# Performance work log

Hardware: AMD Instinct MI355X
Metric: run time of the kernel (lower is better)

## Reference

```python
import jax, jax.numpy as jnp
import numpy as np

S, B, DIN, DBERT, H, L = 128, 32, 256, 768, 512, 2
NT_POS, NT_MORPH = 32, 64


def setup_inputs() -> dict:
    key = jax.random.key(0)
    ks = iter(jax.random.split(key, 32))
    def rn(shape, s=0.1):
        return jax.random.normal(next(ks), shape, dtype=jnp.float32) * s
    D0 = DIN + DBERT  # 1024 == 2*H, so per-layer LSTM weights stack cleanly
    return {
        "src_segments": rn((S, B, DIN), 1.0),
        "bert_encodings": rn((B, DBERT), 1.0),
        "labels_pos": jax.random.randint(next(ks), (S, B), 0, NT_POS, dtype=jnp.int32),
        "labels_morph": jax.random.randint(next(ks), (S, B), 0, NT_MORPH, dtype=jnp.int32),
        # stacked LSTM params: [layer, direction, ...], PyTorch gate order i,f,g,o
        "w_ih": rn((L, 2, 4 * H, D0)),
        "w_hh": rn((L, 2, 4 * H, H)),
        "b_ih": rn((L, 2, 4 * H)),
        "b_hh": rn((L, 2, 4 * H)),
        "head_w_pos": rn((NT_POS, 2 * H)),
        "head_b_pos": rn((NT_POS,)),
        "head_w_morph": rn((NT_MORPH, 2 * H)),
        "head_b_morph": rn((NT_MORPH,)),
        "start_pos": rn((NT_POS,)), "end_pos": rn((NT_POS,)), "trans_pos": rn((NT_POS, NT_POS)),
        "start_morph": rn((NT_MORPH,)), "end_morph": rn((NT_MORPH,)), "trans_morph": rn((NT_MORPH, NT_MORPH)),
    }


def _run_dir(x, w_ih, w_hh, b):
    # x: [S, B, D]; one LSTM direction via scan over time
    bsz, hd = x.shape[1], w_hh.shape[1]
    def step(carry, xt):
        h, c = carry
        g = xt @ w_ih.T + h @ w_hh.T + b  # [B, 4H]
        i, f, gg, o = jnp.split(g, 4, axis=-1)
        c = jax.nn.sigmoid(f) * c + jax.nn.sigmoid(i) * jnp.tanh(gg)
        h = jax.nn.sigmoid(o) * jnp.tanh(c)
        return (h, c), h
    init = (jnp.zeros((bsz, hd), x.dtype), jnp.zeros((bsz, hd), x.dtype))
    _, hs = jax.lax.scan(step, init, x)
    return hs


def _bilstm(x, w_ih, w_hh, b_ih, b_hh):
    out = x
    for l in range(w_ih.shape[0]):
        b = b_ih[l] + b_hh[l]
        fwd = _run_dir(out, w_ih[l, 0], w_hh[l, 0], b[0])
        bwd = _run_dir(out[::-1], w_ih[l, 1], w_hh[l, 1], b[1])[::-1]
        out = jnp.concatenate([fwd, bwd], axis=-1)  # [S, B, 2H]
    return out


def _crf_ll(em, tags, start, trans, end):
    # torchcrf log-likelihood, mask=None, reduction='sum'. em: [S,B,K], tags: [S,B]
    bsz = em.shape[1]
    first = start[tags[0]] + em[0, jnp.arange(bsz), tags[0]]
    em_sc = jnp.take_along_axis(em, tags[..., None], axis=2)[..., 0]  # [S,B]
    num = first + trans[tags[:-1], tags[1:]].sum(0) + em_sc[1:].sum(0) + end[tags[-1]]
    def step(alpha, et):  # alpha: [B,K]
        return jax.nn.logsumexp(alpha[:, :, None] + trans[None], axis=1) + et, None
    alpha, _ = jax.lax.scan(step, start[None, :] + em[0], em[1:])
    den = jax.nn.logsumexp(alpha + end[None, :], axis=1)
    return jnp.sum(num - den)


def reference(src_segments, bert_encodings, labels_pos, labels_morph,
              w_ih, w_hh, b_ih, b_hh,
              head_w_pos, head_b_pos, head_w_morph, head_b_morph,
              start_pos, end_pos, trans_pos, start_morph, end_morph, trans_morph):
    # bert encodings are repeated over seq and concatenated on features
    bert = jnp.broadcast_to(bert_encodings[None], (src_segments.shape[0],) + bert_encodings.shape)
    emb = jnp.concatenate([src_segments, bert], axis=-1)  # dropout p=0 -> identity
    out = _bilstm(emb, w_ih, w_hh, b_ih, b_hh)            # [S,B,2H]
    feat_pos = out @ head_w_pos.T + head_b_pos            # [S,B,32]
    feat_morph = out @ head_w_morph.T + head_b_morph      # [S,B,64]
    ll = (_crf_ll(feat_pos, labels_pos, start_pos, trans_pos, end_pos)
          + _crf_ll(feat_morph, labels_morph, start_morph, trans_morph, end_morph))
    return -ll  # loss = -sum_f crf_f(emissions_f, labels_f)
```

## Files before the change

### kernel.cpp

```cpp
#include <hip/hip_runtime.h>


typedef unsigned short u16;
typedef unsigned int u32;
typedef unsigned long long u64;
typedef __attribute__((ext_vector_type(8))) __bf16 bf16x8;
typedef __attribute__((ext_vector_type(4))) float floatx4;

typedef const __attribute__((address_space(1))) u32 gu32;
typedef __attribute__((address_space(3))) u32 lu32;

static __device__ __forceinline__ u16 f2bf(float f) {
  u32 u = __float_as_uint(f);
  u += 0x7fffu + ((u >> 16) & 1u);
  return (u16)(u >> 16);
}
static __device__ __forceinline__ u64 pack4(float4 v) {
  return (u64)f2bf(v.x) | ((u64)f2bf(v.y) << 16) |
         ((u64)f2bf(v.z) << 32) | ((u64)f2bf(v.w) << 48);
}
static __device__ __forceinline__ float bf2f(u32 bits) {
  return __uint_as_float(bits << 16);
}
static __device__ __forceinline__ float sigf(float x) {
  return 1.0f / (1.0f + __expf(-x));
}
static __device__ __forceinline__ float tanh_(float x) {
  return 1.0f - 2.0f / (1.0f + __expf(2.0f * x));
}
static __device__ __forceinline__ floatx4 mfma16(bf16x8 a, bf16x8 b, floatx4 c) {
  return __builtin_amdgcn_mfma_f32_16x16x32_bf16(a, b, c, 0, 0, 0);
}
static __device__ __forceinline__ u64 aload64(const u64* p) {
  return __hip_atomic_load((u64*)p, __ATOMIC_RELAXED, __HIP_MEMORY_SCOPE_AGENT);
}
static __device__ __forceinline__ void astore64(u64* p, u64 v) {
  __hip_atomic_store(p, v, __ATOMIC_RELAXED, __HIP_MEMORY_SCOPE_AGENT);
}
static __device__ __forceinline__ void gload16(const u16* g, u16* lds_base) {
  __builtin_amdgcn_global_load_lds((gu32*)g, (lu32*)lds_base, 16, 0, 0);
}

__global__ __launch_bounds__(256) void prep_kernel(
    const float* __restrict__ w_ih, const float* __restrict__ w_hh,
    const float* __restrict__ b_ih, const float* __restrict__ b_hh,
    const float* __restrict__ src,  const float* __restrict__ bert,
    const float* __restrict__ hwp,  const float* __restrict__ hbp,
    const float* __restrict__ hwm,  const float* __restrict__ hbm,
    u16* __restrict__ Wsrc, u16* __restrict__ Wbert, u16* __restrict__ Wih1,
    u16* __restrict__ Whh,  u16* __restrict__ SrcBf, u16* __restrict__ BertBf,
    u16* __restrict__ Wheads, float* __restrict__ b0sum, float* __restrict__ b1sum,
    float* __restrict__ hb, float* __restrict__ dout,
    u64* __restrict__ out0s, u64* __restrict__ out1s)
{
  const int A4 = 1048576;
  const int B4 = 1048576;
  const int C4 = 1048576;
  const int D4 = 262144;
  const int E4 = 6144;
  const int F4 = 24576;
  const int G4 = 2048;
  const int H4 = 24;
  const int NI = 2097152;
  const int TOTAL = A4 + B4 + C4 + D4 + E4 + F4 + G4 + H4 + 1 + NI;
  for (int i = blockIdx.x * 256 + threadIdx.x; i < TOTAL; i += gridDim.x * 256) {
    int x = i;
    if (x < A4) {
      const int e = x * 4, c = e & 1023, r = e >> 10;
      const u64 pk = pack4(*(const float4*)&w_ih[e]);
      if (c < 256) *(u64*)&Wsrc[r * 256 + c] = pk;
      else         *(u64*)&Wbert[r * 768 + (c - 256)] = pk;
      continue;
    }
    x -= A4;
    if (x < B4) {
      *(u64*)&Wih1[x * 4] = pack4(*(const float4*)&w_ih[4194304 + x * 4]);
      continue;
    }
    x -= B4;
    if (x < C4) {
      *(u64*)&Whh[x * 4] = pack4(*(const float4*)&w_hh[x * 4]);
      continue;
    }
    x -= C4;
    if (x < D4) {
      *(u64*)&SrcBf[x * 4] = pack4(*(const float4*)&src[x * 4]);
      continue;
    }
    x -= D4;
    if (x < E4) {
      *(u64*)&BertBf[x * 4] = pack4(*(const float4*)&bert[x * 4]);
      continue;
    }
    x -= E4;
    if (x < F4) {
      const int e = x * 4;
      const float4 v = (e < 32768) ? *(const float4*)&hwp[e]
                                   : *(const float4*)&hwm[e - 32768];
      *(u64*)&Wheads[e] = pack4(v);
      continue;
    }
    x -= F4;
    if (x < G4) {
      const int e = x * 4;
      const float4 a = *(const float4*)&b_ih[e];
      const float4 b = *(const float4*)&b_hh[e];
      const float4 v = {a.x + b.x, a.y + b.y, a.z + b.z, a.w + b.w};
      if (e < 4096) *(float4*)&b0sum[e] = v;
      else          *(float4*)&b1sum[e - 4096] = v;
      continue;
    }
    x -= G4;
    if (x < H4) {
      const int e = x * 4;
      const float4 v = (e < 32) ? *(const float4*)&hbp[e]
                                : *(const float4*)&hbm[e - 32];
      *(float4*)&hb[e] = v;
      continue;
    }
    x -= H4;
    if (x == 0) { dout[0] = 0.f; continue; }
    x -= 1;
    if (x < 1048576) out0s[x] = ~0ULL;
    else             out1s[x - 1048576] = ~0ULL;
  }
}

__global__ __launch_bounds__(256) void gemm_nt(
    const u16* __restrict__ A, int lda,
    const u16* __restrict__ B, int ldb,
    float* __restrict__ C, int ldc,
    int M, int N, int K,
    const float* __restrict__ bias_n,
    const float* __restrict__ auxBN, int auxld,
    int mode)
{
  __shared__ __align__(16) u16 As[128 * 64];
  __shared__ __align__(16) u16 Bs[128 * 64];
  const int m0 = blockIdx.y * 128, n0 = blockIdx.x * 128;
  const int tid = threadIdx.x;
  const int wv = tid >> 6, ln = tid & 63;
  const int wm = wv & 1, wn = wv >> 1;
  const int q = ln >> 4, l15 = ln & 15;
  floatx4 acc[4][4];
#pragma unroll
  for (int a = 0; a < 4; ++a)
#pragma unroll
    for (int b2 = 0; b2 < 4; ++b2) acc[a][b2] = (floatx4){0.f, 0.f, 0.f, 0.f};

  for (int kk = 0; kk < K; kk += 64) {
    __syncthreads();
#pragma unroll
    for (int j = 0; j < 4; ++j) {
      const int idx = j * 256 + tid;
      const int r = idx >> 3;
      const int cc = (idx & 7) ^ (r & 7);
      const int cb = __builtin_amdgcn_readfirstlane((j * 256 + wv * 64) * 8);
      const int ra = min(m0 + r, M - 1);
      gload16(&A[(long)ra * lda + kk + cc * 8], &As[cb]);
      const int rb = min(n0 + r, N - 1);
      gload16(&B[(long)rb * ldb + kk + cc * 8], &Bs[cb]);
    }
    __syncthreads();
#pragma unroll
    for (int ks = 0; ks < 2; ++ks) {
      bf16x8 af[4], bf[4];
#pragma unroll
      for (int im = 0; im < 4; ++im) {
        const int r = wm * 64 + im * 16 + l15;
        const int slot = (ks * 4 + q) ^ (r & 7);
        af[im] = *(const bf16x8*)&As[r * 64 + slot * 8];
      }
#pragma unroll
      for (int jn = 0; jn < 4; ++jn) {
        const int r = wn * 64 + jn * 16 + l15;
        const int slot = (ks * 4 + q) ^ (r & 7);
        bf[jn] = *(const bf16x8*)&Bs[r * 64 + slot * 8];
      }
#pragma unroll
      for (int im = 0; im < 4; ++im)
#pragma unroll
        for (int jn = 0; jn < 4; ++jn)
          acc[im][jn] = mfma16(af[im], bf[jn], acc[im][jn]);
    }
  }
  if (mode == 0) {
#pragma unroll
    for (int im = 0; im < 4; ++im)
#pragma unroll
      for (int jn = 0; jn < 4; ++jn) {
        const int n = n0 + wn * 64 + jn * 16 + l15;
        if (n < N) {
          const float badd = bias_n ? bias_n[n] : 0.f;
#pragma unroll
          for (int rg = 0; rg < 4; ++rg) {
            const int m = m0 + wm * 64 + im * 16 + q * 4 + rg;
            if (m < M) {
              float v = acc[im][jn][rg] + badd;
              if (auxBN) v += auxBN[(long)(m & 31) * auxld + n];
              C[(long)m * ldc + n] = v;
            }
          }
        }
      }
  } else {
    u64* G = (u64*)C;
#pragma unroll
    for (int im = 0; im < 4; ++im)
#pragma unroll
      for (int jn = 0; jn < 4; ++jn) {
        const int n = n0 + wn * 64 + jn * 16 + l15;
        const int dirsel = n >> 11, nn = n & 2047;
        const int gt = nn >> 9, u = nn & 511;
        const int ub = u >> 4, low = u & 15;
        const int wvl = low >> 2, jl = low & 3;
        const int l15l = gt * 4 + jl;
        const int m = m0 + wm * 64 + im * 16 + q * 4;
        const int s = m >> 5, b0 = m & 31;
        const int mh = b0 >> 4, qq = (b0 >> 2) & 3;
        const float badd = bias_n ? bias_n[n] : 0.f;
        u64 pk = 0;
#pragma unroll
        for (int rg = 0; rg < 4; ++rg) {
          float v = acc[im][jn][rg] + badd;
          if (auxBN) v += auxBN[(long)(b0 + rg) * auxld + n];
          pk |= (u64)f2bf(v) << (16 * rg);
        }
        G[(((((long)dirsel * 128 + s) * 2 + mh) * 32 + ub) * 4 + wvl) * 64
          + l15l * 4 + qq] = pk;
      }
  }
}

__global__ __launch_bounds__(256, 1) void lstm_rec(
    const u16* __restrict__ gates,
    u16* __restrict__ out,
    const u16* __restrict__ whh)
{
  __shared__ __align__(16) u16 h_lds[16 * 512];
  __shared__ float gsc[4][16][17];
  const int bid = blockIdx.x;
  const int dir = bid >> 6;
  const int mh = (bid >> 5) & 1;
  const int ub = bid & 31;
  const int u0 = ub * 16;
  const int tid = threadIdx.x;
  const int wv = tid >> 6;
  const int ln = tid & 63;
  const int q = ln >> 4, l15 = ln & 15;

  const int gate_r = (l15 >> 2) * 512 + u0 + wv * 4 + (l15 & 3);

  bf16x8 bfrag[16];
  {
    const u16* wp = whh + ((long)dir * 2048 + gate_r) * 512 + q * 8;
#pragma unroll
    for (int ks = 0; ks < 16; ++ks)
      bfrag[ks] = *(const bf16x8*)(wp + ks * 32);
  }

  float c = 0.f;
  const int b_glob = mh * 16 + l15;

  const u64* gbase = (const u64*)gates
      + ((((long)dir * 128 * 2 + mh) * 32 + ub) * 4 + wv) * 64 + l15 * 4 + q;

  u64 gcur = gbase[(long)(dir ? 127 : 0) * 16384];
  u64 gnext = 0;

  for (int t = 0; t < 128; ++t) {
    const int s = dir ? (127 - t) : t;
    if (t < 127) {
      const int sn = dir ? (126 - t) : (t + 1);
      gnext = gbase[(long)sn * 16384];
    }
    floatx4 acc = (floatx4){0.f, 0.f, 0.f, 0.f};
    if (t > 0) {
      const int sp = dir ? (s + 1) : (s - 1);
      const u64* ubp = (const u64*)(out + (((long)sp * 32 + mh * 16) * 1024 + (long)dir * 512));
      u64 v8[8];
#pragma unroll
      for (int j = 0; j < 8; ++j) {
        const int idx = j * 256 + tid;
        const int r = idx >> 7, c4 = idx & 127;
        v8[j] = aload64(ubp + (long)r * 256 + c4);
      }
      while (true) {
        bool bad = false;
#pragma unroll
        for (int j = 0; j < 8; ++j) bad |= ((v8[j] & 0xffffULL) == 0xffffULL);
        if (!bad) break;
#pragma unroll
        for (int j = 0; j < 8; ++j) {
          if ((v8[j] & 0xffffULL) == 0xffffULL) {
            const int idx = j * 256 + tid;
            const int r = idx >> 7, c4 = idx & 127;
            v8[j] = aload64(ubp + (long)r * 256 + c4);
          }
        }
      }
#pragma unroll
      for (int j = 0; j < 8; ++j) {
        const int idx = j * 256 + tid;
        const int r = idx >> 7, c4 = idx & 127;
        const int cc8 = c4 >> 1, hf = c4 & 1;
        *(u64*)&h_lds[r * 512 + ((cc8 ^ (r & 7)) << 3) + (hf << 2)] = v8[j];
      }
      __syncthreads();
      floatx4 acc1 = (floatx4){0.f, 0.f, 0.f, 0.f};
      floatx4 acc2 = (floatx4){0.f, 0.f, 0.f, 0.f};
      floatx4 acc3 = (floatx4){0.f, 0.f, 0.f, 0.f};
#pragma unroll
      for (int ks = 0; ks < 16; ks += 4) {
        const int slot0 = (ks * 4 + q) ^ (l15 & 7);
        bf16x8 a0 = *(const bf16x8*)&h_lds[l15 * 512 + slot0 * 8];
        acc = mfma16(a0, bfrag[ks], acc);
        const int slot1 = ((ks + 1) * 4 + q) ^ (l15 & 7);
        bf16x8 a1 = *(const bf16x8*)&h_lds[l15 * 512 + slot1 * 8];
        acc1 = mfma16(a1, bfrag[ks + 1], acc1);
        const int slot2 = ((ks + 2) * 4 + q) ^ (l15 & 7);
        bf16x8 a2 = *(const bf16x8*)&h_lds[l15 * 512 + slot2 * 8];
        acc2 = mfma16(a2, bfrag[ks + 2], acc2);
        const int slot3 = ((ks + 3) * 4 + q) ^ (l15 & 7);
        bf16x8 a3 = *(const bf16x8*)&h_lds[l15 * 512 + slot3 * 8];
        acc3 = mfma16(a3, bfrag[ks + 3], acc3);
      }
      acc += acc1;
      acc2 += acc3;
      acc += acc2;
    }
#pragma unroll
    for (int rg = 0; rg < 4; ++rg)
      gsc[wv][q * 4 + rg][l15] = acc[rg] + bf2f((u32)((gcur >> (16 * rg)) & 0xffffu));
    const float gi = gsc[wv][l15][q];
    const float gf = gsc[wv][l15][4 + q];
    const float gg = gsc[wv][l15][8 + q];
    const float go = gsc[wv][l15][12 + q];
    const float iv = sigf(gi), fv = sigf(gf), gv = tanh_(gg), ov = sigf(go);
    c = fv * c + iv * gv;
    const float h = ov * tanh_(c);
    const u32 hv = (u32)f2bf(h);
    const u32 p1 = (u32)__shfl_xor((int)hv, 16);
    const u32 lo32 = hv | (p1 << 16);
    const u64 w64 = (u64)lo32 |
                    ((u64)(u32)__shfl_xor((int)lo32, 32) << 32);
    if (q == 0)
      astore64(
          (u64*)&out[((long)s * 32 + b_glob) * 1024 + dir * 512 + u0 + wv * 4],
          w64);
    gcur = gnext;
  }
}

template <int K>
static __device__ void crf_body(const float* __restrict__ feat, int off,
                                const int* __restrict__ labels, int b,
                                const float* __restrict__ start,
                                const float* __restrict__ end_,
                                const float* __restrict__ trans,
                                float* __restrict__ outp,
                                float* transT, float (*alpha)[64],
                                float* red)
{
  const int tid = threadIdx.x;
  for (int i = tid; i < K * K; i += 256) {
    int kk = i / K, kp2 = i % K;
    transT[kp2 * 65 + kk] = trans[i];
  }
  if (tid < K) alpha[0][tid] = start[tid] + feat[b * 96 + off + tid];
  __syncthreads();
  constexpr int Kq = K / 4;
  const int kp = tid >> 2, k4 = tid & 3;
  const bool act = kp < K;
  int p = 0;
  for (int s = 1; s < 128; ++s) {
    float x[Kq];
    float mx = -3e38f;
    if (act) {
      const float* tr = &transT[kp * 65 + k4 * Kq];
      const float* al = &alpha[p][k4 * Kq];
#pragma unroll
      for (int i2 = 0; i2 < Kq; ++i2) { x[i2] = al[i2] + tr[i2]; mx = fmaxf(mx, x[i2]); }
    }
    mx = fmaxf(mx, __shfl_xor(mx, 1));
    mx = fmaxf(mx, __shfl_xor(mx, 2));
    float ss = 0.f;
    if (act) {
#pragma unroll
      for (int i2 = 0; i2 < Kq; ++i2) ss += __expf(x[i2] - mx);
    }
    ss += __shfl_xor(ss, 1);
    ss += __shfl_xor(ss, 2);
    if (act && k4 == 0)
      alpha[p ^ 1][kp] = mx + __logf(ss) + feat[(s * 32 + b) * 96 + off + kp];
    __syncthreads();
    p ^= 1;
  }
  if (tid < 128) {
    const int tg = labels[tid * 32 + b];
    float term = feat[(tid * 32 + b) * 96 + off + tg];
    if (tid == 0) term += start[tg];
    else          term += trans[labels[(tid - 1) * 32 + b] * K + tg];
    if (tid == 127) term += end_[tg];
    red[tid] = term;
  }
  __syncthreads();
  if (tid == 0) {
    float num = 0.f;
    for (int i = 0; i < 128; ++i) num += red[i];
    float mx = -3e38f;
    for (int k = 0; k < K; ++k) mx = fmaxf(mx, alpha[p][k] + end_[k]);
    float ss = 0.f;
    for (int k = 0; k < K; ++k) ss += __expf(alpha[p][k] + end_[k] - mx);
    const float den = mx + __logf(ss);
    atomicAdd(outp, den - num);
  }
}

__global__ __launch_bounds__(256) void crf_kernel(
    const float* __restrict__ feat,
    const int* __restrict__ labp, const int* __restrict__ labm,
    const float* __restrict__ stp, const float* __restrict__ enp, const float* __restrict__ trp,
    const float* __restrict__ stm, const float* __restrict__ enm, const float* __restrict__ trm,
    float* __restrict__ outp)
{
  __shared__ float transT[64 * 65];
  __shared__ float alpha[2][64];
  __shared__ float red[128];
  const int task = blockIdx.x >> 5, b = blockIdx.x & 31;
  if (task == 0) crf_body<32>(feat, 0,  labp, b, stp, enp, trp, outp, transT, alpha, red);
  else           crf_body<64>(feat, 32, labm, b, stm, enm, trm, outp, transT, alpha, red);
}

extern "C" void kernel_launch(void* const* d_in, const int* in_sizes, int n_in,
                              void* d_out, int out_size, void* d_ws, size_t ws_size,
                              hipStream_t stream) {
  const float* src  = (const float*)d_in[0];
  const float* bert = (const float*)d_in[1];
  const int*   labp = (const int*)d_in[2];
  const int*   labm = (const int*)d_in[3];
  const float* w_ih = (const float*)d_in[4];
  const float* w_hh = (const float*)d_in[5];
  const float* b_ih = (const float*)d_in[6];
  const float* b_hh = (const float*)d_in[7];
  const float* hwp  = (const float*)d_in[8];
  const float* hbp  = (const float*)d_in[9];
  const float* hwm  = (const float*)d_in[10];
  const float* hbm  = (const float*)d_in[11];
  const float* stp  = (const float*)d_in[12];
  const float* enp  = (const float*)d_in[13];
  const float* trp  = (const float*)d_in[14];
  const float* stm  = (const float*)d_in[15];
  const float* enm  = (const float*)d_in[16];
  const float* trm  = (const float*)d_in[17];

  char* ws = (char*)d_ws;
  u16*   Wsrc     = (u16*)(ws + 0);
  u16*   Wbert    = (u16*)(ws + 2097152);
  u16*   Wih1     = (u16*)(ws + 8388608);
  u16*   Whh      = (u16*)(ws + 16777216);
  u16*   SrcBf    = (u16*)(ws + 25165824);
  u16*   BertBf   = (u16*)(ws + 27262976);
  u16*   Wheads   = (u16*)(ws + 27312128);
  float* b0sum    = (float*)(ws + 27508736);
  float* b1sum    = (float*)(ws + 27525120);
  float* hb       = (float*)(ws + 27541504);
  float* bertpart = (float*)(ws + 27542272);
  float* feat     = (float*)(ws + 28066560);
  u16*   out0     = (u16*)(ws + 29639424);
  u16*   out1     = (u16*)(ws + 38028032);
  u16*   gates    = (u16*)(ws + 46416640);
  float* dout     = (float*)d_out;

  hipLaunchKernelGGL(prep_kernel, dim3(2048), dim3(256), 0, stream,
      w_ih, w_hh, b_ih, b_hh, src, bert, hwp, hbp, hwm, hbm,
      Wsrc, Wbert, Wih1, Whh, SrcBf, BertBf, Wheads, b0sum, b1sum, hb, dout,
      (u64*)out0, (u64*)out1);

  hipLaunchKernelGGL(gemm_nt, dim3(32, 1), dim3(256), 0, stream,
      BertBf, 768, Wbert, 768, bertpart, 4096, 32, 4096, 768,
      b0sum, (const float*)nullptr, 0, 0);

  hipLaunchKernelGGL(gemm_nt, dim3(32, 32), dim3(256), 0, stream,
      SrcBf, 256, Wsrc, 256, (float*)gates, 0, 4096, 4096, 256,
      (const float*)nullptr, bertpart, 4096, 1);

  {
    const u16* g = gates; u16* o = out0; const u16* wh = Whh;
    void* args[] = {&g, &o, &wh};
    if (hipLaunchCooperativeKernel(reinterpret_cast<void*>(&lstm_rec),
                                   dim3(128), dim3(256), args, 0, stream)
        != hipSuccess) {
      hipLaunchKernelGGL(lstm_rec, dim3(128), dim3(256), 0, stream, g, o, wh);
    }
  }

  hipLaunchKernelGGL(gemm_nt, dim3(32, 32), dim3(256), 0, stream,
      out0, 1024, Wih1, 1024, (float*)gates, 0, 4096, 4096, 1024,
      b1sum, (const float*)nullptr, 0, 1);

  {
    const u16* g = gates; u16* o = out1; const u16* wh = Whh + 2L * 2048 * 512;
    void* args[] = {&g, &o, &wh};
    if (hipLaunchCooperativeKernel(reinterpret_cast<void*>(&lstm_rec),
                                   dim3(128), dim3(256), args, 0, stream)
        != hipSuccess) {
      hipLaunchKernelGGL(lstm_rec, dim3(128), dim3(256), 0, stream, g, o, wh);
    }
  }

  hipLaunchKernelGGL(gemm_nt, dim3(1, 32), dim3(256), 0, stream,
      out1, 1024, Wheads, 1024, feat, 96, 4096, 96, 1024,
      hb, (const float*)nullptr, 0, 0);

  hipLaunchKernelGGL(crf_kernel, dim3(64), dim3(256), 0, stream,
      feat, labp, labm, stp, enp, trp, stm, enm, trm, dout);
}
```

Baseline: 872.3 us.

## Repartition LSTM recurrence into 16 blocks of 1024 threads covering full batch

The recurrent LSTM kernel is restructured from 128 blocks of 256 threads, each handling 16 hidden units for half the batch, to 16 blocks of 1024 threads. Each block now handles 64 hidden units for all 32 batch rows, reusing each W_hh fragment for two MFMA row tiles. The aim is to cut redundant weight residency and the number of blocks polling the cross-block h spin-wait each step. In exchange, each step runs on far fewer CUs, with larger blocks, a bigger LDS footprint and serialized gate processing for the two batch halves.

```diff
diff --git a/kernel.cpp b/kernel.cpp
--- a/kernel.cpp
+++ b/kernel.cpp
@@ -232,24 +232,22 @@
   }
 }
 
-__global__ __launch_bounds__(256, 1) void lstm_rec(
+__global__ __launch_bounds__(1024, 1) void lstm_rec2(
     const u16* __restrict__ gates,
     u16* __restrict__ out,
     const u16* __restrict__ whh)
 {
-  __shared__ __align__(16) u16 h_lds[16 * 512];
-  __shared__ float gsc[4][16][17];
+  __shared__ __align__(16) u16 h_lds[32 * 512];
+  __shared__ float gsc[16][16][17];
   const int bid = blockIdx.x;
-  const int dir = bid >> 6;
-  const int mh = (bid >> 5) & 1;
-  const int ub = bid & 31;
-  const int u0 = ub * 16;
+  const int dir = bid >> 3;
+  const int u8b = bid & 7;
   const int tid = threadIdx.x;
-  const int wv = tid >> 6;
+  const int w = tid >> 6;
   const int ln = tid & 63;
   const int q = ln >> 4, l15 = ln & 15;
 
-  const int gate_r = (l15 >> 2) * 512 + u0 + wv * 4 + (l15 & 3);
+  const int gate_r = (l15 >> 2) * 512 + u8b * 64 + w * 4 + (l15 & 3);
 
   bf16x8 bfrag[16];
   {
@@ -259,96 +257,113 @@
       bfrag[ks] = *(const bf16x8*)(wp + ks * 32);
   }
 
-  float c = 0.f;
-  const int b_glob = mh * 16 + l15;
-
-  const u64* gbase = (const u64*)gates
-      + ((((long)dir * 128 * 2 + mh) * 32 + ub) * 4 + wv) * 64 + l15 * 4 + q;
-
-  u64 gcur = gbase[(long)(dir ? 127 : 0) * 16384];
-  u64 gnext = 0;
+  float c0 = 0.f, c1 = 0.f;
+
+  const u64* gb = (const u64*)gates + (long)dir * 2097152
+      + (long)(u8b * 4 + (w >> 2)) * 256 + (w & 3) * 64 + l15 * 4 + q;
+
+  const long s0 = (long)(dir ? 127 : 0) * 16384;
+  u64 gcur0 = gb[s0];
+  u64 gcur1 = gb[s0 + 8192];
+  u64 gnext0 = 0, gnext1 = 0;
 
   for (int t = 0; t < 128; ++t) {
     const int s = dir ? (127 - t) : t;
     if (t < 127) {
-      const int sn = dir ? (126 - t) : (t + 1);
-      gnext = gbase[(long)sn * 16384];
-    }
-    floatx4 acc = (floatx4){0.f, 0.f, 0.f, 0.f};
+      const long sn = (long)(dir ? (126 - t) : (t + 1)) * 16384;
+      gnext0 = gb[sn];
+      gnext1 = gb[sn + 8192];
+    }
+    floatx4 a0 = (floatx4){0.f, 0.f, 0.f, 0.f};
+    floatx4 b0 = (floatx4){0.f, 0.f, 0.f, 0.f};
     if (t > 0) {
       const int sp = dir ? (s + 1) : (s - 1);
-      const u64* ubp = (const u64*)(out + (((long)sp * 32 + mh * 16) * 1024 + (long)dir * 512));
-      u64 v8[8];
-#pragma unroll
-      for (int j = 0; j < 8; ++j) {
-        const int idx = j * 256 + tid;
+      const u64* ubp = (const u64*)out + (long)sp * 8192 + dir * 128;
+      u64 v4[4];
+#pragma unroll
+      for (int j = 0; j < 4; ++j) {
+        const int idx = j * 1024 + tid;
         const int r = idx >> 7, c4 = idx & 127;
-        v8[j] = aload64(ubp + (long)r * 256 + c4);
+        v4[j] = aload64(ubp + (long)r * 256 + c4);
       }
       while (true) {
         bool bad = false;
 #pragma unroll
-        for (int j = 0; j < 8; ++j) bad |= ((v8[j] & 0xffffULL) == 0xffffULL);
+        for (int j = 0; j < 4; ++j) bad |= ((v4[j] & 0xffffULL) == 0xffffULL);
         if (!bad) break;
 #pragma unroll
-        for (int j = 0; j < 8; ++j) {
-          if ((v8[j] & 0xffffULL) == 0xffffULL) {
-            const int idx = j * 256 + tid;
+        for (int j = 0; j < 4; ++j) {
+          if ((v4[j] & 0xffffULL) == 0xffffULL) {
+            const int idx = j * 1024 + tid;
             const int r = idx >> 7, c4 = idx & 127;
-            v8[j] = aload64(ubp + (long)r * 256 + c4);
+            v4[j] = aload64(ubp + (long)r * 256 + c4);
           }
         }
       }
 #pragma unroll
-      for (int j = 0; j < 8; ++j) {
-        const int idx = j * 256 + tid;
+      for (int j = 0; j < 4; ++j) {
+        const int idx = j * 1024 + tid;
         const int r = idx >> 7, c4 = idx & 127;
         const int cc8 = c4 >> 1, hf = c4 & 1;
-        *(u64*)&h_lds[r * 512 + ((cc8 ^ (r & 7)) << 3) + (hf << 2)] = v8[j];
+        *(u64*)&h_lds[r * 512 + ((cc8 ^ (r & 7)) << 3) + (hf << 2)] = v4[j];
       }
       __syncthreads();
-      floatx4 acc1 = (floatx4){0.f, 0.f, 0.f, 0.f};
-      floatx4 acc2 = (floatx4){0.f, 0.f, 0.f, 0.f};
-      floatx4 acc3 = (floatx4){0.f, 0.f, 0.f, 0.f};
-#pragma unroll
-      for (int ks = 0; ks < 16; ks += 4) {
-        const int slot0 = (ks * 4 + q) ^ (l15 & 7);
-        bf16x8 a0 = *(const bf16x8*)&h_lds[l15 * 512 + slot0 * 8];
-        acc = mfma16(a0, bfrag[ks], acc);
-        const int slot1 = ((ks + 1) * 4 + q) ^ (l15 & 7);
-        bf16x8 a1 = *(const bf16x8*)&h_lds[l15 * 512 + slot1 * 8];
-        acc1 = mfma16(a1, bfrag[ks + 1], acc1);
-        const int slot2 = ((ks + 2) * 4 + q) ^ (l15 & 7);
-        bf16x8 a2 = *(const bf16x8*)&h_lds[l15 * 512 + slot2 * 8];
-        acc2 = mfma16(a2, bfrag[ks + 2], acc2);
-        const int slot3 = ((ks + 3) * 4 + q) ^ (l15 & 7);
-        bf16x8 a3 = *(const bf16x8*)&h_lds[l15 * 512 + slot3 * 8];
-        acc3 = mfma16(a3, bfrag[ks + 3], acc3);
-      }
-      acc += acc1;
-      acc2 += acc3;
-      acc += acc2;
+      floatx4 a1 = (floatx4){0.f, 0.f, 0.f, 0.f};
+      floatx4 b1 = (floatx4){0.f, 0.f, 0.f, 0.f};
+      const u16* row0 = &h_lds[l15 * 512];
+      const u16* row1 = &h_lds[(16 + l15) * 512];
+#pragma unroll
+      for (int ks = 0; ks < 16; ks += 2) {
+        const int sl0 = ((ks * 4 + q) ^ (l15 & 7)) << 3;
+        const int sl1 = (((ks + 1) * 4 + q) ^ (l15 & 7)) << 3;
+        a0 = mfma16(*(const bf16x8*)&row0[sl0], bfrag[ks], a0);
+        b0 = mfma16(*(const bf16x8*)&row1[sl0], bfrag[ks], b0);
+        a1 = mfma16(*(const bf16x8*)&row0[sl1], bfrag[ks + 1], a1);
+        b1 = mfma16(*(const bf16x8*)&row1[sl1], bfrag[ks + 1], b1);
+      }
+      a0 += a1;
+      b0 += b1;
     }
 #pragma unroll
     for (int rg = 0; rg < 4; ++rg)
-      gsc[wv][q * 4 + rg][l15] = acc[rg] + bf2f((u32)((gcur >> (16 * rg)) & 0xffffu));
-    const float gi = gsc[wv][l15][q];
-    const float gf = gsc[wv][l15][4 + q];
-    const float gg = gsc[wv][l15][8 + q];
-    const float go = gsc[wv][l15][12 + q];
-    const float iv = sigf(gi), fv = sigf(gf), gv = tanh_(gg), ov = sigf(go);
-    c = fv * c + iv * gv;
-    const float h = ov * tanh_(c);
-    const u32 hv = (u32)f2bf(h);
-    const u32 p1 = (u32)__shfl_xor((int)hv, 16);
-    const u32 lo32 = hv | (p1 << 16);
-    const u64 w64 = (u64)lo32 |
-                    ((u64)(u32)__shfl_xor((int)lo32, 32) << 32);
-    if (q == 0)
-      astore64(
-          (u64*)&out[((long)s * 32 + b_glob) * 1024 + dir * 512 + u0 + wv * 4],
-          w64);
-    gcur = gnext;
+      gsc[w][q * 4 + rg][l15] = a0[rg] + bf2f((u32)((gcur0 >> (16 * rg)) & 0xffffu));
+    {
+      const float gi = gsc[w][l15][q];
+      const float gf = gsc[w][l15][4 + q];
+      const float gg = gsc[w][l15][8 + q];
+      const float go = gsc[w][l15][12 + q];
+      const float iv = sigf(gi), fv = sigf(gf), gv = tanh_(gg), ov = sigf(go);
+      c0 = fv * c0 + iv * gv;
+      const float h = ov * tanh_(c0);
+      const u32 hv = (u32)f2bf(h);
+      const u32 p1 = (u32)__shfl_xor((int)hv, 16);
+      const u32 lo32 = hv | (p1 << 16);
+      const u64 w64 = (u64)lo32 | ((u64)(u32)__shfl_xor((int)lo32, 32) << 32);
+      if (q == 0)
+        astore64((u64*)&out[((long)s * 32 + l15) * 1024 + dir * 512 + u8b * 64 + w * 4],
+                 w64);
+    }
+#pragma unroll
+    for (int rg = 0; rg < 4; ++rg)
+      gsc[w][q * 4 + rg][l15] = b0[rg] + bf2f((u32)((gcur1 >> (16 * rg)) & 0xffffu));
+    {
+      const float gi = gsc[w][l15][q];
+      const float gf = gsc[w][l15][4 + q];
+      const float gg = gsc[w][l15][8 + q];
+      const float go = gsc[w][l15][12 + q];
+      const float iv = sigf(gi), fv = sigf(gf), gv = tanh_(gg), ov = sigf(go);
+      c1 = fv * c1 + iv * gv;
+      const float h = ov * tanh_(c1);
+      const u32 hv = (u32)f2bf(h);
+      const u32 p1 = (u32)__shfl_xor((int)hv, 16);
+      const u32 lo32 = hv | (p1 << 16);
+      const u64 w64 = (u64)lo32 | ((u64)(u32)__shfl_xor((int)lo32, 32) << 32);
+      if (q == 0)
+        astore64((u64*)&out[((long)s * 32 + 16 + l15) * 1024 + dir * 512 + u8b * 64 + w * 4],
+                 w64);
+    }
+    gcur0 = gnext0;
+    gcur1 = gnext1;
   }
 }
 
@@ -488,10 +503,10 @@
   {
     const u16* g = gates; u16* o = out0; const u16* wh = Whh;
     void* args[] = {&g, &o, &wh};
-    if (hipLaunchCooperativeKernel(reinterpret_cast<void*>(&lstm_rec),
-                                   dim3(128), dim3(256), args, 0, stream)
+    if (hipLaunchCooperativeKernel(reinterpret_cast<void*>(&lstm_rec2),
+                                   dim3(16), dim3(1024), args, 0, stream)
         != hipSuccess) {
-      hipLaunchKernelGGL(lstm_rec, dim3(128), dim3(256), 0, stream, g, o, wh);
+      hipLaunchKernelGGL(lstm_rec2, dim3(16), dim3(1024), 0, stream, g, o, wh);
     }
   }
 
@@ -502,10 +517,10 @@
   {
     const u16* g = gates; u16* o = out1; const u16* wh = Whh + 2L * 2048 * 512;
     void* args[] = {&g, &o, &wh};
-    if (hipLaunchCooperativeKernel(reinterpret_cast<void*>(&lstm_rec),
-                                   dim3(128), dim3(256), args, 0, stream)
+    if (hipLaunchCooperativeKernel(reinterpret_cast<void*>(&lstm_rec2),
+                                   dim3(16), dim3(1024), args, 0, stream)
         != hipSuccess) {
-      hipLaunchKernelGGL(lstm_rec, dim3(128), dim3(256), 0, stream, g, o, wh);
+      hipLaunchKernelGGL(lstm_rec2, dim3(16), dim3(1024), 0, stream, g, o, wh);
     }
   }
 
```

Measured after the change: 3.098 ms. 255% more time.
